# Kernel optimization log

Measured on AMD Instinct MI355X. Metric: run time of the kernel, lower is better.

Reference implementation:

```python
import jax, jax.numpy as jnp
import numpy as np

GAMMA = 12.0
NUM_NODES = 100000


def setup_inputs() -> dict:
    key = jax.random.key(0)
    k1, k2, k3, k4 = jax.random.split(key, 4)
    N, E, D = NUM_NODES, 600000, 128
    node_emb = jax.random.normal(k1, (N, D), dtype=jnp.float32)
    edge_emb = jax.random.normal(k2, (E, D), dtype=jnp.float32)
    src = jax.random.randint(k3, (E,), 0, N, dtype=jnp.int32)
    dst = jax.random.randint(k4, (E,), 0, N, dtype=jnp.int32)
    return {"node_emb": node_emb, "edge_emb": edge_emb, "src": src, "dst": dst}


def reference(node_emb, edge_emb, src, dst):
    # edge_func: score = sigmoid(gamma - ||head + rel - tail||_2), trans = head + rel
    head = node_emb[src]            # [E, D] gather
    tail = node_emb[dst]            # [E, D] gather
    trans = head + edge_emb         # [E, D]
    diff = trans - tail
    dist = jnp.sqrt(jnp.sum(diff * diff, axis=-1))          # [E] L2 norm (dist_ord=2)
    score = jax.nn.sigmoid(GAMMA - dist)                    # [E]
    # reduce_func: h[v] = sum over incoming edges of score * trans
    h = jax.ops.segment_sum(score[:, None] * trans, dst, num_segments=NUM_NODES)
    return h
```

## Files before the change

kernel.cpp:

```cpp
#include <hip/hip_runtime.h>

#define DIM 128
#define GAMMA 12.0f
#define SCAN_BLOCK 256
#define SCAN_ELEMS 1024

__global__ __launch_bounds__(256) void hist_rank_kernel(const int* __restrict__ dst,
                                                        int* __restrict__ cnt,
                                                        int* __restrict__ rank, int E) {
    int e = blockIdx.x * (int)blockDim.x + (int)threadIdx.x;
    if (e < E) rank[e] = atomicAdd(&cnt[dst[e]], 1);
}

__global__ __launch_bounds__(SCAN_BLOCK) void scan_reduce_kernel(
    const int* __restrict__ cnt, int* __restrict__ blockSums, int N) {
    int b = blockIdx.x, t = threadIdx.x;
    int base = b * SCAN_ELEMS + t * 4;
    int s = 0;
    #pragma unroll
    for (int j = 0; j < 4; ++j) {
        int i = base + j;
        if (i < N) s += cnt[i];
    }
    #pragma unroll
    for (int off = 32; off > 0; off >>= 1) s += __shfl_down(s, off, 64);
    __shared__ int wsum[SCAN_BLOCK / 64];
    if ((t & 63) == 0) wsum[t >> 6] = s;
    __syncthreads();
    if (t == 0) {
        int tot = 0;
        #pragma unroll
        for (int w = 0; w < SCAN_BLOCK / 64; ++w) tot += wsum[w];
        blockSums[b] = tot;
    }
}

__global__ __launch_bounds__(SCAN_BLOCK) void scan_spine_kernel(
    int* __restrict__ blockSums, int B) {
    __shared__ int sh[SCAN_BLOCK];
    int t = threadIdx.x;
    int v = (t < B) ? blockSums[t] : 0;
    sh[t] = v;
    __syncthreads();
    for (int off = 1; off < SCAN_BLOCK; off <<= 1) {
        int u = (t >= off) ? sh[t - off] : 0;
        __syncthreads();
        sh[t] += u;
        __syncthreads();
    }
    if (t < B) blockSums[t] = sh[t] - v;
}

__global__ __launch_bounds__(SCAN_BLOCK) void scan_final_kernel(
    const int* __restrict__ blockSums, const int* __restrict__ cnt,
    int* __restrict__ offs, int N) {
    __shared__ int sh[SCAN_BLOCK];
    int b = blockIdx.x, t = threadIdx.x;
    int base = b * SCAN_ELEMS + t * 4;
    int v[4];
    int s = 0;
    #pragma unroll
    for (int j = 0; j < 4; ++j) {
        int i = base + j;
        v[j] = (i < N) ? cnt[i] : 0;
        s += v[j];
    }
    sh[t] = s;
    __syncthreads();
    for (int off = 1; off < SCAN_BLOCK; off <<= 1) {
        int u = (t >= off) ? sh[t - off] : 0;
        __syncthreads();
        sh[t] += u;
        __syncthreads();
    }
    int run = blockSums[b] + sh[t] - s;
    #pragma unroll
    for (int j = 0; j < 4; ++j) {
        int i = base + j;
        if (i < N) offs[i] = run;
        run += v[j];
    }
}

__global__ __launch_bounds__(256) void scatter_pack_kernel(
    const int* __restrict__ dst, const int* __restrict__ src,
    const int* __restrict__ rank, const int* __restrict__ offs,
    int2* __restrict__ sorted2, int E) {
    int e = blockIdx.x * (int)blockDim.x + (int)threadIdx.x;
    if (e < E) {
        int d = dst[e];
        sorted2[offs[d] + rank[e]] = make_int2(e, src[e]);
    }
}

__global__ __launch_bounds__(256) void node_kernel(
    const float* __restrict__ node_emb,
    const float* __restrict__ edge_emb,
    const int2* __restrict__ sorted2,
    const int* __restrict__ offs,
    float* __restrict__ out,
    int N, int E)
{
    int wave = (blockIdx.x * (int)blockDim.x + (int)threadIdx.x) >> 6;
    int lane = (int)threadIdx.x & 63;
    if (wave >= N) return;

    int g  = lane >> 4;
    int gl = lane & 15;

    int start = offs[wave];
    int end   = (wave + 1 < N) ? offs[wave + 1] : E;

    const float4* tp = (const float4*)(node_emb + (size_t)wave * DIM);
    float4 t0 = tp[gl];
    float4 t1 = tp[gl + 16];

    float4 a0 = make_float4(0.f, 0.f, 0.f, 0.f);
    float4 a1 = make_float4(0.f, 0.f, 0.f, 0.f);

    int k = start + g;
    int2 es = (k < end) ? sorted2[k] : make_int2(0, 0);
    while (k < end) {
        int kn = k + 4;
        int2 esn = (kn < end) ? sorted2[kn] : es;

        const float4* hp = (const float4*)(node_emb + (size_t)es.y * DIM);
        const float4* rp = (const float4*)(edge_emb + (size_t)es.x * DIM);
        float4 h0 = hp[gl],      h1 = hp[gl + 16];
        float4 r0 = rp[gl],      r1 = rp[gl + 16];

        float4 x0, x1;
        x0.x = h0.x + r0.x; x0.y = h0.y + r0.y; x0.z = h0.z + r0.z; x0.w = h0.w + r0.w;
        x1.x = h1.x + r1.x; x1.y = h1.y + r1.y; x1.z = h1.z + r1.z; x1.w = h1.w + r1.w;

        float d0, sq;
        d0 = x0.x - t0.x; sq  = d0 * d0;
        d0 = x0.y - t0.y; sq += d0 * d0;
        d0 = x0.z - t0.z; sq += d0 * d0;
        d0 = x0.w - t0.w; sq += d0 * d0;
        d0 = x1.x - t1.x; sq += d0 * d0;
        d0 = x1.y - t1.y; sq += d0 * d0;
        d0 = x1.z - t1.z; sq += d0 * d0;
        d0 = x1.w - t1.w; sq += d0 * d0;

        #pragma unroll
        for (int off = 8; off > 0; off >>= 1)
            sq += __shfl_xor(sq, off, 64);

        float score = 1.0f / (1.0f + expf(sqrtf(sq) - GAMMA));
        a0.x += score * x0.x; a0.y += score * x0.y; a0.z += score * x0.z; a0.w += score * x0.w;
        a1.x += score * x1.x; a1.y += score * x1.y; a1.z += score * x1.z; a1.w += score * x1.w;

        es = esn; k = kn;
    }

    #pragma unroll
    for (int off = 16; off <= 32; off <<= 1) {
        a0.x += __shfl_xor(a0.x, off, 64); a0.y += __shfl_xor(a0.y, off, 64);
        a0.z += __shfl_xor(a0.z, off, 64); a0.w += __shfl_xor(a0.w, off, 64);
        a1.x += __shfl_xor(a1.x, off, 64); a1.y += __shfl_xor(a1.y, off, 64);
        a1.z += __shfl_xor(a1.z, off, 64); a1.w += __shfl_xor(a1.w, off, 64);
    }

    if (g == 0) {
        float4* op = (float4*)(out + (size_t)wave * DIM);
        op[gl]      = a0;
        op[gl + 16] = a1;
    }
}

extern "C" void kernel_launch(void* const* d_in, const int* in_sizes, int n_in,
                              void* d_out, int out_size, void* d_ws, size_t ws_size,
                              hipStream_t stream) {
    const float* node_emb = (const float*)d_in[0];
    const float* edge_emb = (const float*)d_in[1];
    const int*   src      = (const int*)d_in[2];
    const int*   dst      = (const int*)d_in[3];
    float*       out      = (float*)d_out;

    int E = in_sizes[2];
    int N = out_size / DIM;
    int B = (N + SCAN_ELEMS - 1) / SCAN_ELEMS;

    int2* sorted2   = (int2*)d_ws;
    int*  cnt       = (int*)(sorted2 + E);
    int*  offs      = cnt + N;
    int*  rank      = offs + N;
    int*  blockSums = rank + E;

    hipMemsetAsync(cnt, 0, (size_t)N * sizeof(int), stream);
    hist_rank_kernel<<<(E + 255) / 256, 256, 0, stream>>>(dst, cnt, rank, E);
    scan_reduce_kernel<<<B, SCAN_BLOCK, 0, stream>>>(cnt, blockSums, N);
    scan_spine_kernel<<<1, SCAN_BLOCK, 0, stream>>>(blockSums, B);
    scan_final_kernel<<<B, SCAN_BLOCK, 0, stream>>>(blockSums, cnt, offs, N);
    scatter_pack_kernel<<<(E + 255) / 256, 256, 0, stream>>>(dst, src, rank, offs,
                                                             sorted2, E);

    dim3 grid(((size_t)N * 64 + 255) / 256);
    node_kernel<<<grid, 256, 0, stream>>>(node_emb, edge_emb, sorted2, offs,
                                          out, N, E);
}
```

Baseline: 528.2 us.

## Fuse CSR build into one cooperative kernel with grid syncs

Replaces the memset and five preprocessing kernels (histogram, three-stage scan, scatter) with one cooperative kernel that uses grid-wide syncs between phases. The scan is reworked as per-chunk scans of 128 entries, a single-block spine scan, and an add-back pass. The aim is to remove the launch gaps between many small kernels, at the cost of grid.sync barriers and a persistent 1024-block grid that must fit co-resident. The node kernel only has a variable rename.

```diff
diff --git a/kernel.cpp b/kernel.cpp
--- a/kernel.cpp
+++ b/kernel.cpp
@@ -1,93 +1,83 @@
 #include <hip/hip_runtime.h>
+#include <hip/hip_cooperative_groups.h>
+
+namespace cg = cooperative_groups;
 
 #define DIM 128
 #define GAMMA 12.0f
-#define SCAN_BLOCK 256
-#define SCAN_ELEMS 1024
+#define PREP_BLOCKS 1024
+#define PREP_THREADS 256
+#define CHUNK 128
 
-__global__ __launch_bounds__(256) void hist_rank_kernel(const int* __restrict__ dst,
-                                                        int* __restrict__ cnt,
-                                                        int* __restrict__ rank, int E) {
-    int e = blockIdx.x * (int)blockDim.x + (int)threadIdx.x;
-    if (e < E) rank[e] = atomicAdd(&cnt[dst[e]], 1);
-}
+__global__ __launch_bounds__(PREP_THREADS, 4) void prep_kernel(
+    const int* __restrict__ src, const int* __restrict__ dst,
+    int2* __restrict__ sorted2, int* __restrict__ cnt,
+    int* __restrict__ offs, int* __restrict__ rank,
+    int* __restrict__ bsum, int N, int E)
+{
+    cg::grid_group grid = cg::this_grid();
+    const int t   = (int)threadIdx.x;
+    const int tid = (int)blockIdx.x * PREP_THREADS + t;
+    const int nth = (int)gridDim.x * PREP_THREADS;
+    const int nchunks = (N + CHUNK - 1) / CHUNK;
 
-__global__ __launch_bounds__(SCAN_BLOCK) void scan_reduce_kernel(
-    const int* __restrict__ cnt, int* __restrict__ blockSums, int N) {
-    int b = blockIdx.x, t = threadIdx.x;
-    int base = b * SCAN_ELEMS + t * 4;
-    int s = 0;
-    #pragma unroll
-    for (int j = 0; j < 4; ++j) {
-        int i = base + j;
-        if (i < N) s += cnt[i];
-    }
-    #pragma unroll
-    for (int off = 32; off > 0; off >>= 1) s += __shfl_down(s, off, 64);
-    __shared__ int wsum[SCAN_BLOCK / 64];
-    if ((t & 63) == 0) wsum[t >> 6] = s;
-    __syncthreads();
-    if (t == 0) {
-        int tot = 0;
-        #pragma unroll
-        for (int w = 0; w < SCAN_BLOCK / 64; ++w) tot += wsum[w];
-        blockSums[b] = tot;
-    }
-}
+    __shared__ int sh[PREP_THREADS];
 
-__global__ __launch_bounds__(SCAN_BLOCK) void scan_spine_kernel(
-    int* __restrict__ blockSums, int B) {
-    __shared__ int sh[SCAN_BLOCK];
-    int t = threadIdx.x;
-    int v = (t < B) ? blockSums[t] : 0;
-    sh[t] = v;
-    __syncthreads();
-    for (int off = 1; off < SCAN_BLOCK; off <<= 1) {
-        int u = (t >= off) ? sh[t - off] : 0;
+    for (int i = tid; i < N; i += nth) cnt[i] = 0;
+    grid.sync();
+
+    for (int e = tid; e < E; e += nth)
+        rank[e] = atomicAdd(&cnt[dst[e]], 1);
+    grid.sync();
+
+    for (int c = (int)blockIdx.x; c < nchunks; c += (int)gridDim.x) {
+        int i = c * CHUNK + t;
+        int v = 0;
+        if (t < CHUNK && i < N) v = cnt[i];
+        sh[t] = (t < CHUNK) ? v : 0;
         __syncthreads();
-        sh[t] += u;
+        for (int off = 1; off < CHUNK; off <<= 1) {
+            int u = (t >= off && t < CHUNK) ? sh[t - off] : 0;
+            __syncthreads();
+            if (t < CHUNK) sh[t] += u;
+            __syncthreads();
+        }
+        if (t < CHUNK && i < N) offs[i] = sh[t] - v;
+        if (t == CHUNK - 1) bsum[c] = sh[t];
         __syncthreads();
     }
-    if (t < B) blockSums[t] = sh[t] - v;
-}
+    grid.sync();
 
-__global__ __launch_bounds__(SCAN_BLOCK) void scan_final_kernel(
-    const int* __restrict__ blockSums, const int* __restrict__ cnt,
-    int* __restrict__ offs, int N) {
-    __shared__ int sh[SCAN_BLOCK];
-    int b = blockIdx.x, t = threadIdx.x;
-    int base = b * SCAN_ELEMS + t * 4;
-    int v[4];
-    int s = 0;
-    #pragma unroll
-    for (int j = 0; j < 4; ++j) {
-        int i = base + j;
-        v[j] = (i < N) ? cnt[i] : 0;
-        s += v[j];
+    if (blockIdx.x == 0) {
+        int v4[4]; int s = 0;
+        #pragma unroll
+        for (int j = 0; j < 4; ++j) {
+            int idx = t * 4 + j;
+            v4[j] = (idx < nchunks) ? bsum[idx] : 0;
+            s += v4[j];
+        }
+        sh[t] = s;
+        __syncthreads();
+        for (int off = 1; off < PREP_THREADS; off <<= 1) {
+            int u = (t >= off) ? sh[t - off] : 0;
+            __syncthreads();
+            sh[t] += u;
+            __syncthreads();
+        }
+        int run = sh[t] - s;
+        #pragma unroll
+        for (int j = 0; j < 4; ++j) {
+            int idx = t * 4 + j;
+            if (idx < nchunks) bsum[idx] = run;
+            run += v4[j];
+        }
     }
-    sh[t] = s;
-    __syncthreads();
-    for (int off = 1; off < SCAN_BLOCK; off <<= 1) {
-        int u = (t >= off) ? sh[t - off] : 0;
-        __syncthreads();
-        sh[t] += u;
-        __syncthreads();
-    }
-    int run = blockSums[b] + sh[t] - s;
-    #pragma unroll
-    for (int j = 0; j < 4; ++j) {
-        int i = base + j;
-        if (i < N) offs[i] = run;
-        run += v[j];
-    }
-}
+    grid.sync();
 
-__global__ __launch_bounds__(256) void scatter_pack_kernel(
-    const int* __restrict__ dst, const int* __restrict__ src,
-    const int* __restrict__ rank, const int* __restrict__ offs,
-    int2* __restrict__ sorted2, int E) {
-    int e = blockIdx.x * (int)blockDim.x + (int)threadIdx.x;
-    if (e < E) {
+    for (int i = tid; i < N; i += nth) offs[i] += bsum[i / CHUNK];
+    grid.sync();
+
+    for (int e = tid; e < E; e += nth) {
         int d = dst[e];
         sorted2[offs[d] + rank[e]] = make_int2(e, src[e]);
     }
@@ -133,15 +123,15 @@
         x0.x = h0.x + r0.x; x0.y = h0.y + r0.y; x0.z = h0.z + r0.z; x0.w = h0.w + r0.w;
         x1.x = h1.x + r1.x; x1.y = h1.y + r1.y; x1.z = h1.z + r1.z; x1.w = h1.w + r1.w;
 
-        float d0, sq;
-        d0 = x0.x - t0.x; sq  = d0 * d0;
-        d0 = x0.y - t0.y; sq += d0 * d0;
-        d0 = x0.z - t0.z; sq += d0 * d0;
-        d0 = x0.w - t0.w; sq += d0 * d0;
-        d0 = x1.x - t1.x; sq += d0 * d0;
-        d0 = x1.y - t1.y; sq += d0 * d0;
-        d0 = x1.z - t1.z; sq += d0 * d0;
-        d0 = x1.w - t1.w; sq += d0 * d0;
+        float dd, sq;
+        dd = x0.x - t0.x; sq  = dd * dd;
+        dd = x0.y - t0.y; sq += dd * dd;
+        dd = x0.z - t0.z; sq += dd * dd;
+        dd = x0.w - t0.w; sq += dd * dd;
+        dd = x1.x - t1.x; sq += dd * dd;
+        dd = x1.y - t1.y; sq += dd * dd;
+        dd = x1.z - t1.z; sq += dd * dd;
+        dd = x1.w - t1.w; sq += dd * dd;
 
         #pragma unroll
         for (int off = 8; off > 0; off >>= 1)
@@ -180,21 +170,19 @@
 
     int E = in_sizes[2];
     int N = out_size / DIM;
-    int B = (N + SCAN_ELEMS - 1) / SCAN_ELEMS;
 
-    int2* sorted2   = (int2*)d_ws;
-    int*  cnt       = (int*)(sorted2 + E);
-    int*  offs      = cnt + N;
-    int*  rank      = offs + N;
-    int*  blockSums = rank + E;
+    int2* sorted2 = (int2*)d_ws;
+    int*  cnt     = (int*)(sorted2 + E);
+    int*  offs    = cnt + N;
+    int*  rank    = offs + N;
+    int*  bsum    = rank + E;
 
-    hipMemsetAsync(cnt, 0, (size_t)N * sizeof(int), stream);
-    hist_rank_kernel<<<(E + 255) / 256, 256, 0, stream>>>(dst, cnt, rank, E);
-    scan_reduce_kernel<<<B, SCAN_BLOCK, 0, stream>>>(cnt, blockSums, N);
-    scan_spine_kernel<<<1, SCAN_BLOCK, 0, stream>>>(blockSums, B);
-    scan_final_kernel<<<B, SCAN_BLOCK, 0, stream>>>(blockSums, cnt, offs, N);
-    scatter_pack_kernel<<<(E + 255) / 256, 256, 0, stream>>>(dst, src, rank, offs,
-                                                             sorted2, E);
+    void* args[] = {(void*)&src, (void*)&dst, (void*)&sorted2, (void*)&cnt,
+                    (void*)&offs, (void*)&rank, (void*)&bsum,
+                    (void*)&N, (void*)&E};
+    hipLaunchCooperativeKernel(reinterpret_cast<void*>(prep_kernel),
+                               dim3(PREP_BLOCKS), dim3(PREP_THREADS),
+                               args, 0, stream);
 
     dim3 grid(((size_t)N * 64 + 255) / 256);
     node_kernel<<<grid, 256, 0, stream>>>(node_emb, edge_emb, sorted2, offs,
```

New measurement: 978.9 us. 1.85x slower.
